# Performance work log

Hardware: AMD Instinct MI355X
Metric: run time of the kernel (lower is better)

## Reference

```python
import jax, jax.numpy as jnp
import numpy as np

DIM_M = 4
DIM_C = 4   # context dim
DIM_F = 4   # feature dim
DIM_Q = DIM_F + 1  # [scale | features]
B = 2_000_000


def setup_inputs() -> dict:
    key = jax.random.key(0)
    k1, k2, k3, k4 = jax.random.split(key, 4)
    xss = jax.random.normal(k1, (B, DIM_M, DIM_Q), dtype=jnp.float32)
    # ragged lengths in [1, DIM_M]
    seq_lengths = jax.random.randint(k2, (B,), 1, DIM_M + 1, dtype=jnp.int64)
    # torch.nn.Linear default init ~ U(-1/sqrt(fan_in), 1/sqrt(fan_in)); any small init is fine for a reference
    W_cob = jax.random.normal(k3, (DIM_C, DIM_F), dtype=jnp.float32) / np.sqrt(DIM_F).astype(np.float32)
    W_reg = jax.random.normal(k4, (DIM_M, DIM_C), dtype=jnp.float32) / np.sqrt(DIM_C).astype(np.float32)
    return {"xss": xss, "seq_lengths": seq_lengths, "W_cob": W_cob, "W_reg": W_reg}


def reference(xss, seq_lengths, W_cob, W_reg):
    # xss: [B, S, Q] with S = DIM_M, Q = DIM_F + 1
    scales = xss[..., 0:1]            # [B, S, 1]
    fs = xss[..., 1:]                 # [B, S, F]
    bs = jnp.einsum('bsf,cf->bsc', fs, W_cob)          # change_of_basis (no bias)
    valid = jnp.arange(DIM_M)[None, :] < seq_lengths[:, None]   # [B, S] ragged mask
    cs = bs * scales * valid[..., None].astype(bs.dtype)        # base_coordinates, masked
    context = cs.sum(axis=1)                                    # pool over valid prefix -> [B, C]
    ys = jnp.einsum('bc,mc->bm', context, W_reg)
    projs = jnp.einsum('bsm,bm->bs', bs, ys)                    # per-position dot with broadcast ys
    # ragged concat: only valid positions, in batch-major order (matches torch.cat of per-batch slices)
    return projs[valid][:, None]                                # [sum(seq_lengths), 1]
```

## Files before the change

### kernel.cpp

```cpp
#include <hip/hip_runtime.h>

#define NT 256

__global__ __launch_bounds__(NT) void sum_kernel(const int* __restrict__ seq,
                                                 unsigned* __restrict__ blockSums,
                                                 int n) {
    __shared__ unsigned red[NT];
    int tid = threadIdx.x;
    int gid = blockIdx.x * NT + tid;
    unsigned L = (gid < n) ? (unsigned)seq[gid] : 0u;
    red[tid] = L;
    __syncthreads();
    #pragma unroll
    for (int s = NT / 2; s > 0; s >>= 1) {
        if (tid < s) red[tid] += red[tid + s];
        __syncthreads();
    }
    if (tid == 0) blockSums[blockIdx.x] = red[0];
}

__global__ __launch_bounds__(NT) void scan_kernel(const unsigned* __restrict__ blockSums,
                                                  unsigned* __restrict__ blockOffsets,
                                                  int nb) {
    __shared__ unsigned sdata[NT];
    int tid = threadIdx.x;
    unsigned carry = 0;
    for (int base = 0; base < nb; base += NT) {
        int i = base + tid;
        unsigned v = (i < nb) ? blockSums[i] : 0u;
        sdata[tid] = v;
        __syncthreads();
        for (int off = 1; off < NT; off <<= 1) {
            unsigned add = (tid >= off) ? sdata[tid - off] : 0u;
            __syncthreads();
            sdata[tid] += add;
            __syncthreads();
        }
        unsigned incl = sdata[tid];
        if (i < nb) blockOffsets[i] = incl - v + carry;
        unsigned tot = sdata[NT - 1];
        __syncthreads();
        carry += tot;
    }
}

__global__ __launch_bounds__(NT) void main_kernel(const float* __restrict__ xss,
                                                  const int* __restrict__ seq,
                                                  const float* __restrict__ Wcob,
                                                  const float* __restrict__ Wreg,
                                                  const unsigned* __restrict__ blockOffsets,
                                                  float* __restrict__ out,
                                                  int n) {
    __shared__ unsigned sscan[NT];
    int tid = threadIdx.x;
    int gid = blockIdx.x * NT + tid;
    unsigned L = (gid < n) ? (unsigned)seq[gid] : 0u;

    sscan[tid] = L;
    __syncthreads();
    for (int off = 1; off < NT; off <<= 1) {
        unsigned add = (tid >= off) ? sscan[tid - off] : 0u;
        __syncthreads();
        sscan[tid] += add;
        __syncthreads();
    }
    unsigned offset = blockOffsets[blockIdx.x] + sscan[tid] - L;

    if (gid >= n) return;

    const float* p = xss + (size_t)gid * 20;
    float4 v0 = *(const float4*)(p + 0);
    float4 v1 = *(const float4*)(p + 4);
    float4 v2 = *(const float4*)(p + 8);
    float4 v3 = *(const float4*)(p + 12);
    float4 v4 = *(const float4*)(p + 16);
    float x[20];
    x[0]=v0.x;  x[1]=v0.y;  x[2]=v0.z;  x[3]=v0.w;
    x[4]=v1.x;  x[5]=v1.y;  x[6]=v1.z;  x[7]=v1.w;
    x[8]=v2.x;  x[9]=v2.y;  x[10]=v2.z; x[11]=v2.w;
    x[12]=v3.x; x[13]=v3.y; x[14]=v3.z; x[15]=v3.w;
    x[16]=v4.x; x[17]=v4.y; x[18]=v4.z; x[19]=v4.w;

    float wc[16], wr[16];
    #pragma unroll
    for (int i = 0; i < 16; i++) { wc[i] = Wcob[i]; wr[i] = Wreg[i]; }

    float bs[4][4];
    #pragma unroll
    for (int s = 0; s < 4; s++) {
        #pragma unroll
        for (int c = 0; c < 4; c++) {
            float acc = 0.f;
            #pragma unroll
            for (int f = 0; f < 4; f++) acc += x[s * 5 + 1 + f] * wc[c * 4 + f];
            bs[s][c] = acc;
        }
    }

    float ctx[4] = {0.f, 0.f, 0.f, 0.f};
    #pragma unroll
    for (int s = 0; s < 4; s++) {
        float m = (s < (int)L) ? x[s * 5] : 0.f;
        #pragma unroll
        for (int c = 0; c < 4; c++) ctx[c] += bs[s][c] * m;
    }

    float ys[4];
    #pragma unroll
    for (int m = 0; m < 4; m++) {
        float acc = 0.f;
        #pragma unroll
        for (int c = 0; c < 4; c++) acc += ctx[c] * wr[m * 4 + c];
        ys[m] = acc;
    }

    #pragma unroll
    for (int s = 0; s < 4; s++) {
        if (s < (int)L) {
            float acc = 0.f;
            #pragma unroll
            for (int m = 0; m < 4; m++) acc += bs[s][m] * ys[m];
            out[offset + s] = acc;
        }
    }
}

extern "C" void kernel_launch(void* const* d_in, const int* in_sizes, int n_in,
                              void* d_out, int out_size, void* d_ws, size_t ws_size,
                              hipStream_t stream) {
    const float* xss  = (const float*)d_in[0];
    const int*   seq  = (const int*)d_in[1];
    const float* Wcob = (const float*)d_in[2];
    const float* Wreg = (const float*)d_in[3];
    float* out = (float*)d_out;

    int n  = in_sizes[1];
    int nb = (n + NT - 1) / NT;

    unsigned* blockSums    = (unsigned*)d_ws;
    unsigned* blockOffsets = blockSums + nb;

    sum_kernel<<<nb, NT, 0, stream>>>(seq, blockSums, n);
    scan_kernel<<<1, NT, 0, stream>>>(blockSums, blockOffsets, nb);
    main_kernel<<<nb, NT, 0, stream>>>(xss, seq, Wcob, Wreg, blockOffsets, out, n);
}
```

Measured before the change: 275.2 us.

## Replace serial single-block scan with hierarchical multi-block scan and wave-shuffle reductions

Replaces the single-block scan over ~7800 block sums, which loops serially with many syncthreads, by a two-level scan: a per-group scan kernel across many blocks plus a tiny single-wave top scan. Block reductions and scans in the sum and main kernels now use 64-lane wave shuffles instead of LDS tree loops. This cuts the serial latency of the scan stage and the barrier count in every block, at the cost of an extra kernel launch. The top scan assumes at most 64 groups.

```diff
diff --git a/kernel.cpp b/kernel.cpp
--- a/kernel.cpp
+++ b/kernel.cpp
@@ -5,43 +5,63 @@
 __global__ __launch_bounds__(NT) void sum_kernel(const int* __restrict__ seq,
                                                  unsigned* __restrict__ blockSums,
                                                  int n) {
-    __shared__ unsigned red[NT];
+    __shared__ unsigned wsum[4];
     int tid = threadIdx.x;
     int gid = blockIdx.x * NT + tid;
-    unsigned L = (gid < n) ? (unsigned)seq[gid] : 0u;
-    red[tid] = L;
+    int lane = tid & 63, wave = tid >> 6;
+    unsigned v = (gid < n) ? (unsigned)seq[gid] : 0u;
+    #pragma unroll
+    for (int off = 32; off > 0; off >>= 1) v += __shfl_down(v, off);
+    if (lane == 0) wsum[wave] = v;
     __syncthreads();
-    #pragma unroll
-    for (int s = NT / 2; s > 0; s >>= 1) {
-        if (tid < s) red[tid] += red[tid + s];
-        __syncthreads();
-    }
-    if (tid == 0) blockSums[blockIdx.x] = red[0];
+    if (tid == 0) blockSums[blockIdx.x] = wsum[0] + wsum[1] + wsum[2] + wsum[3];
 }
 
-__global__ __launch_bounds__(NT) void scan_kernel(const unsigned* __restrict__ blockSums,
-                                                  unsigned* __restrict__ blockOffsets,
-                                                  int nb) {
-    __shared__ unsigned sdata[NT];
+__device__ __forceinline__ unsigned block_excl_scan(unsigned v_in, int tid,
+                                                    unsigned* wtot ,
+                                                    unsigned* block_total) {
+    int lane = tid & 63, wave = tid >> 6;
+    unsigned v = v_in;
+    #pragma unroll
+    for (int off = 1; off < 64; off <<= 1) {
+        unsigned t = __shfl_up(v, off);
+        if (lane >= off) v += t;
+    }
+    if (lane == 63) wtot[wave] = v;
+    __syncthreads();
+    unsigned woff = 0;
+    #pragma unroll
+    for (int w = 0; w < 4; w++) woff += (w < wave) ? wtot[w] : 0u;
+    if (block_total) *block_total = wtot[0] + wtot[1] + wtot[2] + wtot[3];
+    return woff + v - v_in;
+}
+
+__global__ __launch_bounds__(NT) void group_scan_kernel(const unsigned* __restrict__ blockSums,
+                                                        unsigned* __restrict__ blockOffsets,
+                                                        unsigned* __restrict__ groupSums,
+                                                        int nb) {
+    __shared__ unsigned wtot[4];
     int tid = threadIdx.x;
-    unsigned carry = 0;
-    for (int base = 0; base < nb; base += NT) {
-        int i = base + tid;
-        unsigned v = (i < nb) ? blockSums[i] : 0u;
-        sdata[tid] = v;
-        __syncthreads();
-        for (int off = 1; off < NT; off <<= 1) {
-            unsigned add = (tid >= off) ? sdata[tid - off] : 0u;
-            __syncthreads();
-            sdata[tid] += add;
-            __syncthreads();
-        }
-        unsigned incl = sdata[tid];
-        if (i < nb) blockOffsets[i] = incl - v + carry;
-        unsigned tot = sdata[NT - 1];
-        __syncthreads();
-        carry += tot;
+    int i = blockIdx.x * NT + tid;
+    unsigned v = (i < nb) ? blockSums[i] : 0u;
+    unsigned total;
+    unsigned excl = block_excl_scan(v, tid, wtot, &total);
+    if (i < nb) blockOffsets[i] = excl;
+    if (tid == 0) groupSums[blockIdx.x] = total;
+}
+
+__global__ __launch_bounds__(64) void top_scan_kernel(const unsigned* __restrict__ groupSums,
+                                                      unsigned* __restrict__ groupOffsets,
+                                                      int ng) {
+    int tid = threadIdx.x;
+    unsigned v = (tid < ng) ? groupSums[tid] : 0u;
+    unsigned incl = v;
+    #pragma unroll
+    for (int off = 1; off < 64; off <<= 1) {
+        unsigned t = __shfl_up(incl, off);
+        if (tid >= off) incl += t;
     }
+    if (tid < ng) groupOffsets[tid] = incl - v;
 }
 
 __global__ __launch_bounds__(NT) void main_kernel(const float* __restrict__ xss,
@@ -49,22 +69,16 @@
                                                   const float* __restrict__ Wcob,
                                                   const float* __restrict__ Wreg,
                                                   const unsigned* __restrict__ blockOffsets,
+                                                  const unsigned* __restrict__ groupOffsets,
                                                   float* __restrict__ out,
                                                   int n) {
-    __shared__ unsigned sscan[NT];
+    __shared__ unsigned wtot[4];
     int tid = threadIdx.x;
     int gid = blockIdx.x * NT + tid;
     unsigned L = (gid < n) ? (unsigned)seq[gid] : 0u;
 
-    sscan[tid] = L;
-    __syncthreads();
-    for (int off = 1; off < NT; off <<= 1) {
-        unsigned add = (tid >= off) ? sscan[tid - off] : 0u;
-        __syncthreads();
-        sscan[tid] += add;
-        __syncthreads();
-    }
-    unsigned offset = blockOffsets[blockIdx.x] + sscan[tid] - L;
+    unsigned excl = block_excl_scan(L, tid, wtot, nullptr);
+    unsigned offset = groupOffsets[blockIdx.x >> 8] + blockOffsets[blockIdx.x] + excl;
 
     if (gid >= n) return;
 
@@ -136,11 +150,15 @@
 
     int n  = in_sizes[1];
     int nb = (n + NT - 1) / NT;
+    int ng = (nb + NT - 1) / NT;
 
     unsigned* blockSums    = (unsigned*)d_ws;
     unsigned* blockOffsets = blockSums + nb;
+    unsigned* groupSums    = blockOffsets + nb;
+    unsigned* groupOffsets = groupSums + ng;
 
     sum_kernel<<<nb, NT, 0, stream>>>(seq, blockSums, n);
-    scan_kernel<<<1, NT, 0, stream>>>(blockSums, blockOffsets, nb);
-    main_kernel<<<nb, NT, 0, stream>>>(xss, seq, Wcob, Wreg, blockOffsets, out, n);
+    group_scan_kernel<<<ng, NT, 0, stream>>>(blockSums, blockOffsets, groupSums, nb);
+    top_scan_kernel<<<1, 64, 0, stream>>>(groupSums, groupOffsets, ng);
+    main_kernel<<<nb, NT, 0, stream>>>(xss, seq, Wcob, Wreg, blockOffsets, groupOffsets, out, n);
 }
```

After: 243.7 us. 1.13x faster.
